# Performance work log

Hardware: AMD Instinct MI355X
Metric: run time of the kernel (lower is better)

Reference implementation:

```python
import jax, jax.numpy as jnp
import numpy as np

N_NODES = 50000


def _gcn_norm(edge_index, num_nodes):
    """PyG GCNConv normalization: add self-loops, symmetric deg^{-1/2} weights."""
    loops = jnp.arange(num_nodes, dtype=edge_index.dtype)
    src = jnp.concatenate([edge_index[0], loops])
    dst = jnp.concatenate([edge_index[1], loops])
    deg = jax.ops.segment_sum(jnp.ones_like(dst, dtype=jnp.float32), dst,
                              num_segments=num_nodes)
    dinv = jax.lax.rsqrt(jnp.maximum(deg, 1.0))  # self-loops guarantee deg>=1
    norm = dinv[src] * dinv[dst]                 # [E + N]
    return src, dst, norm


def _gcn_conv(x, W, b, src, dst, norm, num_nodes):
    h = x @ W                                    # [N, out] dense GEMM
    msg = h[src] * norm[:, None]                 # gather + scale
    agg = jax.ops.segment_sum(msg, dst, num_segments=num_nodes)
    return agg + b


def setup_inputs() -> dict:
    key = jax.random.key(0)
    ks = jax.random.split(key, 8)
    d = 128
    scale = 1.0 / np.sqrt(d)
    emb = jax.random.normal(ks[0], (N_NODES, d), dtype=jnp.float32)
    W1 = jax.random.normal(ks[1], (d, d), dtype=jnp.float32) * scale
    W2 = jax.random.normal(ks[2], (d, d), dtype=jnp.float32) * scale
    W3 = jax.random.normal(ks[3], (d, d), dtype=jnp.float32) * scale
    b1 = jnp.zeros((d,), dtype=jnp.float32)
    b2 = jnp.zeros((d,), dtype=jnp.float32)
    b3 = jnp.zeros((d,), dtype=jnp.float32)
    edge_index = jax.random.randint(ks[4], (2, 600000), 0, N_NODES, dtype=jnp.int64)
    return {"emb": emb, "W1": W1, "b1": b1, "W2": W2, "b2": b2,
            "W3": W3, "b3": b3, "edge_index": edge_index}


def reference(emb, W1, b1, W2, b2, W3, b3, edge_index):
    # Eval-mode forward: F.dropout(training=False) is identity.
    src, dst, norm = _gcn_norm(edge_index, N_NODES)
    x = emb
    x = jax.nn.relu(_gcn_conv(x, W1, b1, src, dst, norm, N_NODES))
    x = jax.nn.relu(_gcn_conv(x, W2, b2, src, dst, norm, N_NODES))
    x = _gcn_conv(x, W3, b3, src, dst, norm, N_NODES)
    x = x.at[0].set(0.0)  # x[0] = zeros(x.shape[1])
    return x
```

## Files before the change

kernel.cpp:

```cpp
#include <hip/hip_runtime.h>
#include <hip/hip_fp16.h>

#define NN 50000
#define D 128
#define STRIDE 64

typedef __attribute__((ext_vector_type(16))) float f32x16;
typedef _Float16 h16;
typedef __attribute__((ext_vector_type(2))) _Float16 h16x2;
typedef __attribute__((ext_vector_type(8))) _Float16 h16x8;

struct alignas(16) H8 { h16 h[8]; };


__global__ __launch_bounds__(256) void fill_kernel(const int* __restrict__ srcA,
                                                   const int* __restrict__ dstA,
                                                   int* __restrict__ cnt,
                                                   int* __restrict__ slots, int nquad) {
    int t = blockIdx.x * 256 + threadIdx.x;
    if (t >= nquad) return;
    int4 s4 = ((const int4*)srcA)[t];
    int4 d4 = ((const int4*)dstA)[t];
    int p0 = atomicAdd(&cnt[d4.x], 1);
    int p1 = atomicAdd(&cnt[d4.y], 1);
    int p2 = atomicAdd(&cnt[d4.z], 1);
    int p3 = atomicAdd(&cnt[d4.w], 1);
    if (p0 < STRIDE - 4) slots[d4.x * STRIDE + p0] = s4.x;
    if (p1 < STRIDE - 4) slots[d4.y * STRIDE + p1] = s4.y;
    if (p2 < STRIDE - 4) slots[d4.z * STRIDE + p2] = s4.z;
    if (p3 < STRIDE - 4) slots[d4.w * STRIDE + p3] = s4.w;
}

__global__ __launch_bounds__(256) void dinv_kernel(const int* __restrict__ cnt,
                                                   float* __restrict__ dinv) {
    int i = blockIdx.x * 256 + threadIdx.x;
    if (i < NN) dinv[i] = rsqrtf((float)cnt[i] + 1.0f);
}

__global__ __launch_bounds__(256) void weight_kernel(const int* __restrict__ cnt,
                                                     const float* __restrict__ dinv,
                                                     const int* __restrict__ slots,
                                                     int2* __restrict__ csr2) {
    int idx = blockIdx.x * 256 + threadIdx.x;
    int node = idx >> 6;
    int j = idx & 63;
    if (node >= NN) return;
    int c = cnt[node];
    int pc = min((c + 4) & ~3, STRIDE);
    if (j < pc) {
        int2 v;
        if (j < c) {
            int s = slots[idx];
            v = make_int2(s, __float_as_int(dinv[s]));
        } else if (j == c) {
            v = make_int2(node, __float_as_int(dinv[node]));
        } else {
            v = make_int2(0, 0);
        }
        csr2[idx] = v;
    }
}

__global__ __launch_bounds__(256, 2) void gemm_mfma(const void* __restrict__ Xv, int x_is_f32,
                                                    const float* __restrict__ W,
                                                    h16* __restrict__ H, int M,
                                                    int* __restrict__ cnt_zero) {
    __shared__ h16 Ws[32768];
    {
        const int l  = threadIdx.x & 63;
        const int ct = threadIdx.x >> 6;
        const int n  = ct * 32 + (l & 31);
        const int lh = l >> 5;
#pragma unroll
        for (int ks = 0; ks < 8; ks++) {
            const int kbase = ks * 16 + lh * 8;
            H8 hi8, lo8;
#pragma unroll
            for (int j = 0; j < 8; j++) {
                float w = W[(kbase + j) * D + n];
                h16 hi = (h16)w;
                hi8.h[j] = hi;
                lo8.h[j] = (h16)(w - (float)hi);
            }
            const int base = ((ks * 4 + ct) * 64 + l) * 8;
            *(H8*)(Ws + base)         = hi8;
            *(H8*)(Ws + base + 16384) = lo8;
        }
        if (cnt_zero && blockIdx.x < 196) {
            int i = blockIdx.x * 256 + threadIdx.x;
            if (i < NN) cnt_zero[i] = 0;
        }
    }
    __syncthreads();

    const int wave = threadIdx.x >> 6;
    const int lane = threadIdx.x & 63;
    const int row0 = blockIdx.x * 128 + wave * 32;
    const int arow = min(row0 + (lane & 31), M - 1);
    const int koff = (lane >> 5) * 8;

    f32x16 acc[4] = {};

#pragma unroll
    for (int ks = 0; ks < 8; ks++) {
        h16x8 ahi, alo;
        if (x_is_f32) {
            const float* p = (const float*)Xv + (size_t)arow * D + koff + ks * 16;
            float4 fa = *(const float4*)p;
            float4 fb = *(const float4*)(p + 4);
            float f[8] = {fa.x, fa.y, fa.z, fa.w, fb.x, fb.y, fb.z, fb.w};
#pragma unroll
            for (int j = 0; j < 8; j++) {
                h16 hi = (h16)f[j];
                ahi[j] = hi;
                alo[j] = (h16)(f[j] - (float)hi);
            }
        } else {
            const h16* p = (const h16*)Xv + (size_t)arow * D + koff + ks * 16;
            ahi = *(const h16x8*)p;
        }
#pragma unroll
        for (int ct = 0; ct < 4; ct++) {
            const int base = ((ks * 4 + ct) * 64 + lane) * 8;
            h16x8 bhi = *(const h16x8*)(Ws + base);
            h16x8 blo = *(const h16x8*)(Ws + base + 16384);
            acc[ct] = __builtin_amdgcn_mfma_f32_32x32x16_f16(ahi, bhi, acc[ct], 0, 0, 0);
            acc[ct] = __builtin_amdgcn_mfma_f32_32x32x16_f16(ahi, blo, acc[ct], 0, 0, 0);
            if (x_is_f32)
                acc[ct] = __builtin_amdgcn_mfma_f32_32x32x16_f16(alo, bhi, acc[ct], 0, 0, 0);
        }
    }

    const int col0 = lane & 31;
    const int rbase = row0 + 4 * (lane >> 5);
#pragma unroll
    for (int ct = 0; ct < 4; ct++) {
#pragma unroll
        for (int r = 0; r < 16; r++) {
            int row = rbase + (r & 3) + 8 * (r >> 2);
            if (row < M) H[(size_t)row * D + ct * 32 + col0] = (h16)acc[ct][r];
        }
    }
}

__global__ __launch_bounds__(256) void agg_kernel(const h16* __restrict__ H,
                                                  const float* __restrict__ dinv,
                                                  const int* __restrict__ cnt,
                                                  const int2* __restrict__ csr2,
                                                  const float* __restrict__ bias,
                                                  h16* __restrict__ out16,
                                                  float* __restrict__ out32,
                                                  int n, int mode) {
    int node = blockIdx.x * 4 + (threadIdx.x >> 6);
    if (node >= n) return;
    int lane = threadIdx.x & 63;
    int col = lane * 2;

    float ax = 0.f, ay = 0.f, bx = 0.f, by = 0.f;

    int c = __builtin_amdgcn_readfirstlane(cnt[node]);
    int s = node * STRIDE;
    int e = s + min((c + 4) & ~3, STRIDE);

    for (int p = s; p < e; p += 4) {
        int2 w0 = csr2[p];
        int2 w1 = csr2[p + 1];
        int2 w2 = csr2[p + 2];
        int2 w3 = csr2[p + 3];
        h16x2 v0 = *(const h16x2*)(H + (size_t)w0.x * D + col);
        h16x2 v1 = *(const h16x2*)(H + (size_t)w1.x * D + col);
        h16x2 v2 = *(const h16x2*)(H + (size_t)w2.x * D + col);
        h16x2 v3 = *(const h16x2*)(H + (size_t)w3.x * D + col);
        float f0 = __int_as_float(w0.y), f1 = __int_as_float(w1.y);
        float f2 = __int_as_float(w2.y), f3 = __int_as_float(w3.y);
        ax = fmaf(f0, (float)v0[0], ax); ay = fmaf(f0, (float)v0[1], ay);
        bx = fmaf(f1, (float)v1[0], bx); by = fmaf(f1, (float)v1[1], by);
        ax = fmaf(f2, (float)v2[0], ax); ay = fmaf(f2, (float)v2[1], ay);
        bx = fmaf(f3, (float)v3[0], bx); by = fmaf(f3, (float)v3[1], by);
    }
    ax += bx; ay += by;

    float di = dinv[node];
    float2 bb = *(const float2*)(bias + col);
    float rx = fmaf(di, ax, bb.x);
    float ry = fmaf(di, ay, bb.y);
    if (mode == 0) {
        rx = fmaxf(rx, 0.f); ry = fmaxf(ry, 0.f);
        h16x2 o; o[0] = (h16)rx; o[1] = (h16)ry;
        *(h16x2*)(out16 + (size_t)node * D + col) = o;
    } else {
        if (node == 0) { rx = 0.f; ry = 0.f; }
        *(float2*)(out32 + (size_t)node * D + col) = make_float2(rx, ry);
    }
}


extern "C" void kernel_launch(void* const* d_in, const int* in_sizes, int n_in,
                              void* d_out, int out_size, void* d_ws, size_t ws_size,
                              hipStream_t stream) {
    const float* emb = (const float*)d_in[0];
    const float* W1  = (const float*)d_in[1];
    const float* b1  = (const float*)d_in[2];
    const float* W2  = (const float*)d_in[3];
    const float* b2  = (const float*)d_in[4];
    const float* W3  = (const float*)d_in[5];
    const float* b3  = (const float*)d_in[6];
    const int*   ei  = (const int*)d_in[7];

    const int E = in_sizes[7] / 2;
    const int* srcA = ei;
    const int* dstA = ei + E;
    float* out = (float*)d_out;

    char* ws = (char*)d_ws;
    size_t off = 0;
    auto alloc = [&](size_t bytes) -> void* {
        void* p = ws + off;
        off = (off + bytes + 255) & ~(size_t)255;
        return p;
    };
    h16* h      = (h16*)alloc((size_t)NN * D * 2);
    h16* x16    = (h16*)alloc((size_t)NN * D * 2);
    float* dinv = (float*)alloc((size_t)NN * 4);
    int* cnt    = (int*)alloc((size_t)NN * 4);
    int* slots  = (int*)alloc((size_t)NN * STRIDE * 4);
    int2* csr2  = (int2*)alloc((size_t)NN * STRIDE * 8);

    const int T = 256;
    const int gemm_grid = (NN + 127) / 128;
    const int agg_grid  = (NN + 3) / 4;
    const int nquad = E / 4;

    gemm_mfma<<<gemm_grid, T, 0, stream>>>(emb, 1, W1, h, NN, cnt);
    fill_kernel<<<(nquad + T - 1) / T, T, 0, stream>>>(srcA, dstA, cnt, slots, nquad);
    dinv_kernel<<<(NN + T - 1) / T, T, 0, stream>>>(cnt, dinv);
    weight_kernel<<<(NN * STRIDE + T - 1) / T, T, 0, stream>>>(cnt, dinv, slots, csr2);
    agg_kernel<<<agg_grid, T, 0, stream>>>(h, dinv, cnt, csr2, b1, x16, nullptr, NN, 0);
    gemm_mfma<<<gemm_grid, T, 0, stream>>>(x16, 0, W2, h, NN, nullptr);
    agg_kernel<<<agg_grid, T, 0, stream>>>(h, dinv, cnt, csr2, b2, x16, nullptr, NN, 0);
    gemm_mfma<<<gemm_grid, T, 0, stream>>>(x16, 0, W3, h, NN, nullptr);
    agg_kernel<<<agg_grid, T, 0, stream>>>(h, dinv, cnt, csr2, b3, nullptr, out, NN, 1);
}
```

Baseline: 262.0 us.

## Precompute split-fp16 weights once, drop dinv/weight kernels, widen aggregation per lane

A small prep kernel converts all three weight matrices into the hi/lo fp16 MFMA layout once and zeroes the degree counters. The GEMM then copies the prepared weights straight into LDS with global_load_lds instead of converting them in every block. The separate dinv and csr2 weight-building kernels are removed. Aggregation reads the slot table directly and computes rsqrt of neighbor degrees on the fly. Each half-wave now handles one node with 4 halfs per lane, which cuts launches and the csr2 write/read traffic in exchange for extra cnt gathers and rsqrt work inside each of the three aggregation passes.

```diff
diff --git a/kernel.cpp b/kernel.cpp
--- a/kernel.cpp
+++ b/kernel.cpp
@@ -7,11 +7,42 @@
 
 typedef __attribute__((ext_vector_type(16))) float f32x16;
 typedef _Float16 h16;
-typedef __attribute__((ext_vector_type(2))) _Float16 h16x2;
+typedef __attribute__((ext_vector_type(4))) _Float16 h16x4;
 typedef __attribute__((ext_vector_type(8))) _Float16 h16x8;
 
 struct alignas(16) H8 { h16 h[8]; };
 
+typedef const __attribute__((address_space(1))) void gvoid;
+typedef __attribute__((address_space(3))) void lvoid;
+
+__global__ __launch_bounds__(256) void wprep_kernel(const float* __restrict__ W1,
+                                                    const float* __restrict__ W2,
+                                                    const float* __restrict__ W3,
+                                                    h16* __restrict__ Wsp,
+                                                    int* __restrict__ cnt) {
+    const float* W = blockIdx.x == 0 ? W1 : (blockIdx.x == 1 ? W2 : W3);
+    h16* dst = Wsp + blockIdx.x * 32768;
+    const int l  = threadIdx.x & 63;
+    const int ct = threadIdx.x >> 6;
+    const int n  = ct * 32 + (l & 31);
+    const int lh = l >> 5;
+#pragma unroll
+    for (int ks = 0; ks < 8; ks++) {
+        const int kbase = ks * 16 + lh * 8;
+        H8 hi8, lo8;
+#pragma unroll
+        for (int j = 0; j < 8; j++) {
+            float w = W[(kbase + j) * D + n];
+            h16 hi = (h16)w;
+            hi8.h[j] = hi;
+            lo8.h[j] = (h16)(w - (float)hi);
+        }
+        const int base = ((ks * 4 + ct) * 64 + l) * 8;
+        *(H8*)(dst + base)         = hi8;
+        *(H8*)(dst + base + 16384) = lo8;
+    }
+    for (int i = blockIdx.x * 256 + threadIdx.x; i < NN; i += 768) cnt[i] = 0;
+}
 
 __global__ __launch_bounds__(256) void fill_kernel(const int* __restrict__ srcA,
                                                    const int* __restrict__ dstA,
@@ -31,64 +62,17 @@
     if (p3 < STRIDE - 4) slots[d4.w * STRIDE + p3] = s4.w;
 }
 
-__global__ __launch_bounds__(256) void dinv_kernel(const int* __restrict__ cnt,
-                                                   float* __restrict__ dinv) {
-    int i = blockIdx.x * 256 + threadIdx.x;
-    if (i < NN) dinv[i] = rsqrtf((float)cnt[i] + 1.0f);
-}
-
-__global__ __launch_bounds__(256) void weight_kernel(const int* __restrict__ cnt,
-                                                     const float* __restrict__ dinv,
-                                                     const int* __restrict__ slots,
-                                                     int2* __restrict__ csr2) {
-    int idx = blockIdx.x * 256 + threadIdx.x;
-    int node = idx >> 6;
-    int j = idx & 63;
-    if (node >= NN) return;
-    int c = cnt[node];
-    int pc = min((c + 4) & ~3, STRIDE);
-    if (j < pc) {
-        int2 v;
-        if (j < c) {
-            int s = slots[idx];
-            v = make_int2(s, __float_as_int(dinv[s]));
-        } else if (j == c) {
-            v = make_int2(node, __float_as_int(dinv[node]));
-        } else {
-            v = make_int2(0, 0);
-        }
-        csr2[idx] = v;
-    }
-}
-
 __global__ __launch_bounds__(256, 2) void gemm_mfma(const void* __restrict__ Xv, int x_is_f32,
-                                                    const float* __restrict__ W,
-                                                    h16* __restrict__ H, int M,
-                                                    int* __restrict__ cnt_zero) {
+                                                    const h16* __restrict__ Wsp,
+                                                    h16* __restrict__ H, int M) {
     __shared__ h16 Ws[32768];
     {
-        const int l  = threadIdx.x & 63;
-        const int ct = threadIdx.x >> 6;
-        const int n  = ct * 32 + (l & 31);
-        const int lh = l >> 5;
-#pragma unroll
-        for (int ks = 0; ks < 8; ks++) {
-            const int kbase = ks * 16 + lh * 8;
-            H8 hi8, lo8;
-#pragma unroll
-            for (int j = 0; j < 8; j++) {
-                float w = W[(kbase + j) * D + n];
-                h16 hi = (h16)w;
-                hi8.h[j] = hi;
-                lo8.h[j] = (h16)(w - (float)hi);
-            }
-            const int base = ((ks * 4 + ct) * 64 + l) * 8;
-            *(H8*)(Ws + base)         = hi8;
-            *(H8*)(Ws + base + 16384) = lo8;
-        }
-        if (cnt_zero && blockIdx.x < 196) {
-            int i = blockIdx.x * 256 + threadIdx.x;
-            if (i < NN) cnt_zero[i] = 0;
+        const int t = threadIdx.x;
+#pragma unroll
+        for (int i = 0; i < 16; i++) {
+            const int off = (i * 256 + t) * 8;
+            __builtin_amdgcn_global_load_lds((gvoid*)(Wsp + off), (lvoid*)(Ws + off),
+                                             16, 0, 0);
         }
     }
     __syncthreads();
@@ -144,53 +128,62 @@
 }
 
 __global__ __launch_bounds__(256) void agg_kernel(const h16* __restrict__ H,
-                                                  const float* __restrict__ dinv,
                                                   const int* __restrict__ cnt,
-                                                  const int2* __restrict__ csr2,
+                                                  const int* __restrict__ slots,
                                                   const float* __restrict__ bias,
                                                   h16* __restrict__ out16,
                                                   float* __restrict__ out32,
-                                                  int n, int mode) {
-    int node = blockIdx.x * 4 + (threadIdx.x >> 6);
-    if (node >= n) return;
-    int lane = threadIdx.x & 63;
-    int col = lane * 2;
-
-    float ax = 0.f, ay = 0.f, bx = 0.f, by = 0.f;
-
-    int c = __builtin_amdgcn_readfirstlane(cnt[node]);
-    int s = node * STRIDE;
-    int e = s + min((c + 4) & ~3, STRIDE);
-
-    for (int p = s; p < e; p += 4) {
-        int2 w0 = csr2[p];
-        int2 w1 = csr2[p + 1];
-        int2 w2 = csr2[p + 2];
-        int2 w3 = csr2[p + 3];
-        h16x2 v0 = *(const h16x2*)(H + (size_t)w0.x * D + col);
-        h16x2 v1 = *(const h16x2*)(H + (size_t)w1.x * D + col);
-        h16x2 v2 = *(const h16x2*)(H + (size_t)w2.x * D + col);
-        h16x2 v3 = *(const h16x2*)(H + (size_t)w3.x * D + col);
-        float f0 = __int_as_float(w0.y), f1 = __int_as_float(w1.y);
-        float f2 = __int_as_float(w2.y), f3 = __int_as_float(w3.y);
-        ax = fmaf(f0, (float)v0[0], ax); ay = fmaf(f0, (float)v0[1], ay);
-        bx = fmaf(f1, (float)v1[0], bx); by = fmaf(f1, (float)v1[1], by);
-        ax = fmaf(f2, (float)v2[0], ax); ay = fmaf(f2, (float)v2[1], ay);
-        bx = fmaf(f3, (float)v3[0], bx); by = fmaf(f3, (float)v3[1], by);
-    }
-    ax += bx; ay += by;
-
-    float di = dinv[node];
-    float2 bb = *(const float2*)(bias + col);
-    float rx = fmaf(di, ax, bb.x);
-    float ry = fmaf(di, ay, bb.y);
+                                                  int mode) {
+    const int lane = threadIdx.x & 63;
+    const int node = blockIdx.x * 8 + ((threadIdx.x >> 6) << 1) + (lane >> 5);
+    const int col  = (lane & 31) * 4;
+
+    const int c = cnt[node];
+    const float di = rsqrtf((float)c + 1.0f);
+    const int sbase = node * STRIDE;
+    const int pc = min((c + 4) & ~3, STRIDE);
+
+    float a0 = 0.f, a1 = 0.f, a2 = 0.f, a3 = 0.f;
+    float c0 = 0.f, c1 = 0.f, c2 = 0.f, c3 = 0.f;
+
+    for (int p = 0; p < pc; p += 4) {
+        int4 s4 = *(const int4*)(slots + sbase + p);
+        int src0 = (p + 0 < c) ? s4.x : node;
+        int src1 = (p + 1 < c) ? s4.y : node;
+        int src2 = (p + 2 < c) ? s4.z : node;
+        int src3 = (p + 3 < c) ? s4.w : node;
+        float w0 = (p + 0 < c) ? rsqrtf((float)cnt[src0] + 1.0f) : ((p + 0 == c) ? di : 0.f);
+        float w1 = (p + 1 < c) ? rsqrtf((float)cnt[src1] + 1.0f) : ((p + 1 == c) ? di : 0.f);
+        float w2 = (p + 2 < c) ? rsqrtf((float)cnt[src2] + 1.0f) : ((p + 2 == c) ? di : 0.f);
+        float w3 = (p + 3 < c) ? rsqrtf((float)cnt[src3] + 1.0f) : ((p + 3 == c) ? di : 0.f);
+        h16x4 v0 = *(const h16x4*)(H + (size_t)src0 * D + col);
+        h16x4 v1 = *(const h16x4*)(H + (size_t)src1 * D + col);
+        h16x4 v2 = *(const h16x4*)(H + (size_t)src2 * D + col);
+        h16x4 v3 = *(const h16x4*)(H + (size_t)src3 * D + col);
+        a0 = fmaf(w0, (float)v0[0], a0); a1 = fmaf(w0, (float)v0[1], a1);
+        a2 = fmaf(w0, (float)v0[2], a2); a3 = fmaf(w0, (float)v0[3], a3);
+        c0 = fmaf(w1, (float)v1[0], c0); c1 = fmaf(w1, (float)v1[1], c1);
+        c2 = fmaf(w1, (float)v1[2], c2); c3 = fmaf(w1, (float)v1[3], c3);
+        a0 = fmaf(w2, (float)v2[0], a0); a1 = fmaf(w2, (float)v2[1], a1);
+        a2 = fmaf(w2, (float)v2[2], a2); a3 = fmaf(w2, (float)v2[3], a3);
+        c0 = fmaf(w3, (float)v3[0], c0); c1 = fmaf(w3, (float)v3[1], c1);
+        c2 = fmaf(w3, (float)v3[2], c2); c3 = fmaf(w3, (float)v3[3], c3);
+    }
+    a0 += c0; a1 += c1; a2 += c2; a3 += c3;
+
+    float4 bb = *(const float4*)(bias + col);
+    float r0 = fmaf(di, a0, bb.x);
+    float r1 = fmaf(di, a1, bb.y);
+    float r2 = fmaf(di, a2, bb.z);
+    float r3 = fmaf(di, a3, bb.w);
     if (mode == 0) {
-        rx = fmaxf(rx, 0.f); ry = fmaxf(ry, 0.f);
-        h16x2 o; o[0] = (h16)rx; o[1] = (h16)ry;
-        *(h16x2*)(out16 + (size_t)node * D + col) = o;
+        h16x4 o;
+        o[0] = (h16)fmaxf(r0, 0.f); o[1] = (h16)fmaxf(r1, 0.f);
+        o[2] = (h16)fmaxf(r2, 0.f); o[3] = (h16)fmaxf(r3, 0.f);
+        *(h16x4*)(out16 + (size_t)node * D + col) = o;
     } else {
-        if (node == 0) { rx = 0.f; ry = 0.f; }
-        *(float2*)(out32 + (size_t)node * D + col) = make_float2(rx, ry);
+        if (node == 0) { r0 = r1 = r2 = r3 = 0.f; }
+        *(float4*)(out32 + (size_t)node * D + col) = make_float4(r0, r1, r2, r3);
     }
 }
 
@@ -221,23 +214,21 @@
     };
     h16* h      = (h16*)alloc((size_t)NN * D * 2);
     h16* x16    = (h16*)alloc((size_t)NN * D * 2);
-    float* dinv = (float*)alloc((size_t)NN * 4);
     int* cnt    = (int*)alloc((size_t)NN * 4);
     int* slots  = (int*)alloc((size_t)NN * STRIDE * 4);
-    int2* csr2  = (int2*)alloc((size_t)NN * STRIDE * 8);
+    h16* Wsp    = (h16*)alloc((size_t)3 * 32768 * 2);
 
     const int T = 256;
     const int gemm_grid = (NN + 127) / 128;
-    const int agg_grid  = (NN + 3) / 4;
+    const int agg_grid  = NN / 8;
     const int nquad = E / 4;
 
-    gemm_mfma<<<gemm_grid, T, 0, stream>>>(emb, 1, W1, h, NN, cnt);
+    wprep_kernel<<<3, T, 0, stream>>>(W1, W2, W3, Wsp, cnt);
+    gemm_mfma<<<gemm_grid, T, 0, stream>>>(emb, 1, Wsp, h, NN);
     fill_kernel<<<(nquad + T - 1) / T, T, 0, stream>>>(srcA, dstA, cnt, slots, nquad);
-    dinv_kernel<<<(NN + T - 1) / T, T, 0, stream>>>(cnt, dinv);
-    weight_kernel<<<(NN * STRIDE + T - 1) / T, T, 0, stream>>>(cnt, dinv, slots, csr2);
-    agg_kernel<<<agg_grid, T, 0, stream>>>(h, dinv, cnt, csr2, b1, x16, nullptr, NN, 0);
-    gemm_mfma<<<gemm_grid, T, 0, stream>>>(x16, 0, W2, h, NN, nullptr);
-    agg_kernel<<<agg_grid, T, 0, stream>>>(h, dinv, cnt, csr2, b2, x16, nullptr, NN, 0);
-    gemm_mfma<<<gemm_grid, T, 0, stream>>>(x16, 0, W3, h, NN, nullptr);
-    agg_kernel<<<agg_grid, T, 0, stream>>>(h, dinv, cnt, csr2, b3, nullptr, out, NN, 1);
-}
+    agg_kernel<<<agg_grid, T, 0, stream>>>(h, cnt, slots, b1, x16, nullptr, 0);
+    gemm_mfma<<<gemm_grid, T, 0, stream>>>(x16, 0, Wsp + 32768, h, NN);
+    agg_kernel<<<agg_grid, T, 0, stream>>>(h, cnt, slots, b2, x16, nullptr, 0);
+    gemm_mfma<<<gemm_grid, T, 0, stream>>>(x16, 0, Wsp + 65536, h, NN);
+    agg_kernel<<<agg_grid, T, 0, stream>>>(h, cnt, slots, b3, nullptr, out, 1);
+}
```

Result: slower. 278.4 us (+6.2%).
